# Kernel optimization log

Hardware: AMD Instinct MI355X
Metric: run time of the kernel (lower is better)

The kernel has to match this reference:

```python
import jax, jax.numpy as jnp
import numpy as np

B, LQ, LK, D = 16, 2048, 2048, 64
TEMPERATURE = 8.0


def setup_inputs() -> dict:
    key = jax.random.key(0)
    kq, kk, kv, kt, km = jax.random.split(key, 5)
    q = jax.random.normal(kq, (B, LQ, D), dtype=jnp.float32)
    k = jax.random.normal(kk, (B, LK, D), dtype=jnp.float32)
    v = jax.random.normal(kv, (B, LK, D), dtype=jnp.float32)
    # time differences are positive
    time_diff = jax.random.uniform(kt, (B, LQ, LK), dtype=jnp.float32)
    mask = jax.random.randint(km, (B, LQ, LK), 0, 2).astype(bool)
    time_plus_weight = jnp.zeros((1,), dtype=jnp.float32)
    time_mul_weight = jnp.ones((1,), dtype=jnp.float32)
    return {"q": q, "k": k, "v": v, "time_diff": time_diff, "mask": mask,
            "time_plus_weight": time_plus_weight, "time_mul_weight": time_mul_weight}


def reference(q, k, v, time_diff, mask, time_plus_weight, time_mul_weight):
    # attn = QK^T / temperature  -> [B, LQ, LK]
    attn = jnp.einsum("bqd,bkd->bqk", q, k) / TEMPERATURE
    # time-decay bias (global mean/max over the whole time_diff tensor)
    td = time_diff / jnp.mean(time_diff)
    td = td + jax.nn.softplus(time_plus_weight) * jnp.max(td)
    time_diff_weight = 1.0 / jnp.log(jnp.exp(jnp.float32(1.0)) + td)
    attn = attn + time_mul_weight * time_diff_weight
    attn = jnp.where(mask, jnp.float32(-1e10), attn)
    attn = jax.nn.softmax(attn, axis=2)
    # dropout is identity in eval / p-effective-0 reference
    output = jnp.einsum("bqk,bkd->bqd", attn, v)
    return (output, attn)
```

## Files before the change

kernel.cpp:

```cpp
#include <hip/hip_runtime.h>
#include <hip/hip_bf16.h>

#define B_N 16
#define LQ_N 2048
#define LK_N 2048
#define D_N 64

typedef __attribute__((ext_vector_type(8))) __bf16 bf16x8;
typedef __attribute__((ext_vector_type(4))) float f32x4;
typedef __attribute__((ext_vector_type(2))) unsigned u32x2;
typedef __attribute__((ext_vector_type(4))) unsigned u32x4;

__device__ __forceinline__ unsigned cvt_pk_bf16(float lo, float hi) {
  unsigned r;
  asm("v_cvt_pk_bf16_f32 %0, %1, %2" : "=v"(r) : "v"(lo), "v"(hi));
  return r;
}

__device__ __forceinline__ void gl_lds16(const float* g, float* l) {
  __builtin_amdgcn_global_load_lds(
      (const __attribute__((address_space(1))) void*)g,
      (__attribute__((address_space(3))) void*)l, 16, 0, 0);
}

#define WAIT_VMC(N)  do { asm volatile("s_waitcnt vmcnt(" #N ")" ::: "memory"); __builtin_amdgcn_sched_barrier(0); } while (0)
#define WAIT_LGKM0() do { asm volatile("s_waitcnt lgkmcnt(0)" ::: "memory");    __builtin_amdgcn_sched_barrier(0); } while (0)
#define SBAR()       __builtin_amdgcn_sched_barrier(0)

__global__ __launch_bounds__(256) void red1_kernel(const float* __restrict__ td,
                                                   float* __restrict__ ws) {
  const int tid = threadIdx.x;
  const int gid = blockIdx.x * 256 + tid;
  float s = 0.f, mx = -1e30f;
  const float4* p = reinterpret_cast<const float4*>(td);
  for (int i = gid; i < 16777216; i += 524288) {
    float4 x = p[i];
    s += (x.x + x.y) + (x.z + x.w);
    mx = fmaxf(mx, fmaxf(fmaxf(x.x, x.y), fmaxf(x.z, x.w)));
  }
#pragma unroll
  for (int m = 1; m < 64; m <<= 1) {
    s += __shfl_xor(s, m, 64);
    mx = fmaxf(mx, __shfl_xor(mx, m, 64));
  }
  __shared__ float ss[4], sm[4];
  if ((tid & 63) == 0) { ss[tid >> 6] = s; sm[tid >> 6] = mx; }
  __syncthreads();
  if (tid == 0) {
    ws[blockIdx.x]        = (ss[0] + ss[1]) + (ss[2] + ss[3]);
    ws[2048 + blockIdx.x] = fmaxf(fmaxf(sm[0], sm[1]), fmaxf(sm[2], sm[3]));
  }
}

__global__ __launch_bounds__(256) void red2_kernel(const float* __restrict__ tpw,
                                                   const unsigned* __restrict__ mku,
                                                   float* __restrict__ ws) {
  const int tid = threadIdx.x;
  double s = 0.0; float mx = -1e30f;
  for (int i = tid; i < 2048; i += 256) { s += (double)ws[i]; mx = fmaxf(mx, ws[2048 + i]); }
#pragma unroll
  for (int m = 1; m < 64; m <<= 1) {
    s += __shfl_xor(s, m, 64);
    mx = fmaxf(mx, __shfl_xor(mx, m, 64));
  }
  unsigned big = 0;
  for (int i = tid; i < 1024; i += 256) big |= (mku[i] > 1u) ? 1u : 0u;
  const int anyw = __any(big != 0);
  __shared__ double sd[4]; __shared__ float sm[4]; __shared__ int sa[4];
  if ((tid & 63) == 0) { sd[tid >> 6] = s; sm[tid >> 6] = mx; sa[tid >> 6] = anyw; }
  __syncthreads();
  if (tid == 0) {
    double tot = (sd[0] + sd[1]) + (sd[2] + sd[3]);
    float m4 = fmaxf(fmaxf(sm[0], sm[1]), fmaxf(sm[2], sm[3]));
    double mean = tot / 67108864.0;
    float inv_mean = (float)(1.0 / mean);
    float sp = log1pf(__expf(tpw[0]));
    ws[4096] = inv_mean;
    ws[4097] = sp * m4 * inv_mean;
    ws[4098] = (sa[0] | sa[1] | sa[2] | sa[3]) ? 1.f : 0.f;
    ws[4099] = 2.718281828459045f + sp * m4 * inv_mean;
  }
}

__global__ __launch_bounds__(1024)
void attn_kernel(
    const float* __restrict__ q, const float* __restrict__ kp, const float* __restrict__ vp,
    const float* __restrict__ td, const unsigned char* __restrict__ maskb,
    const float* __restrict__ tmwp, const float* __restrict__ ws,
    float* __restrict__ out, float* __restrict__ attn) {

  __shared__ float regA[16][2][1024];
  __shared__ unsigned short Qsb[16 * 72];
  __shared__ unsigned short Ps[16][16 * 24];
  __shared__ float rsum[16][16];

  const int tid  = threadIdx.x;
  const int w    = tid >> 6;
  const int lane = tid & 63;
  const int lrow = lane & 15;
  const int lgrp = lane >> 4;

  const int b     = blockIdx.x >> 7;
  const int qbase = (blockIdx.x & 127) << 4;

  const float inv_mean = ws[4096];
  const float ec       = ws[4099];
  const float tmw      = tmwp[0];
  const float sc       = tmw * 2.0813689810056077f;
  const int   msh      = (ws[4098] != 0.f) ? 0 : 2;

  if (tid < 256) {
    const float qscale = 0.18033688011112042f;
    const int row = tid >> 4, c4 = (tid & 15) << 2;
    f32x4 x = *reinterpret_cast<const f32x4*>(q + ((size_t)(b * LQ_N + qbase + row) << 6) + c4);
    *reinterpret_cast<u32x2*>(&Qsb[row * 72 + c4]) =
        u32x2{ cvt_pk_bf16(x[0] * qscale, x[1] * qscale),
               cvt_pk_bf16(x[2] * qscale, x[3] * qscale) };
  }
  __syncthreads();

  const unsigned qrow = (unsigned)(b * LQ_N + qbase + lrow);
  const unsigned tdo0 = (qrow << 11) + (unsigned)(w * 16 + lgrp * 4);
  const unsigned kvo0 = ((unsigned)b << 17) + ((unsigned)w << 10);
  const unsigned pA = (lgrp << 6) + ((lrow ^ lgrp)       << 2);
  const unsigned pB = (lgrp << 6) + ((lrow ^ (lgrp + 4)) << 2);

  auto dma16 = [&](const float* src_base, int c, int pb) {
    const unsigned base = kvo0 + (unsigned)c * 16384u;
    gl_lds16(src_base + (base         + pA), &regA[w][pb][0]);
    gl_lds16(src_base + (base +  256u + pB), &regA[w][pb][256]);
    gl_lds16(src_base + (base +  512u + pA), &regA[w][pb][512]);
    gl_lds16(src_base + (base +  768u + pB), &regA[w][pb][768]);
  };

  auto ldtd = [&](int c, f32x4* tdv, unsigned* mk4) {
    const unsigned to = tdo0 + (unsigned)c * 256u;
    *tdv = __builtin_nontemporal_load(reinterpret_cast<const f32x4*>(td + to));
    if (msh == 0) {
      *mk4 = *reinterpret_cast<const unsigned*>(maskb + to);
    } else {
      u32x4 m = __builtin_nontemporal_load(
          reinterpret_cast<const u32x4*>(maskb + ((size_t)to << 2)));
      *mk4 = (m[0] & 1u) | ((m[1] & 1u) << 8) | ((m[2] & 1u) << 16) | ((m[3] & 1u) << 24);
    }
  };

  dma16(kp, 0, 0); SBAR();
  dma16(kp, 1, 1); SBAR();
  f32x4    tdb[2];
  unsigned mkb[2];
  ldtd(0, &tdb[0], &mkb[0]); SBAR();

  float rs = 0.f;
  u32x2 E[8];

#pragma unroll
  for (int c = 0; c < 8; ++c) {
    if (c == 0)      { WAIT_VMC(5); }
    else if (c <= 6) { WAIT_VMC(6); }
    else             { WAIT_VMC(2); }

    f32x4 acc = {0.f, 0.f, 0.f, 0.f};
#pragma unroll
    for (int h = 0; h < 2; ++h) {
      const int g0 = (h * 8 + lgrp * 2 + 0) ^ (lrow & 7);
      const int g1 = (h * 8 + lgrp * 2 + 1) ^ (lrow & 7);
      f32x4 ka = *(const f32x4*)&regA[w][c & 1][lrow * 64 + g0 * 4];
      f32x4 kc = *(const f32x4*)&regA[w][c & 1][lrow * 64 + g1 * 4];
      bf16x8 qv = *(const bf16x8*)&Qsb[lrow * 72 + h * 32 + lgrp * 8];
      u32x4 kd = { cvt_pk_bf16(ka[0], ka[1]), cvt_pk_bf16(ka[2], ka[3]),
                   cvt_pk_bf16(kc[0], kc[1]), cvt_pk_bf16(kc[2], kc[3]) };
      acc = __builtin_amdgcn_mfma_f32_16x16x32_bf16(__builtin_bit_cast(bf16x8, kd), qv,
                                                    acc, 0, 0, 0);
    }
    WAIT_LGKM0();
    if (c < 6) { dma16(kp, c + 2, c & 1); SBAR(); }
    if (c < 7) { ldtd(c + 1, &tdb[(c + 1) & 1], &mkb[(c + 1) & 1]); SBAR(); }

    if (c <= 5)      { WAIT_VMC(5); }
    else if (c == 6) { WAIT_VMC(1); }
    else             { WAIT_VMC(0); }

    const f32x4    tv  = tdb[c & 1];
    const unsigned mk4 = mkb[c & 1];
    float e4[4];
#pragma unroll
    for (int i = 0; i < 4; ++i) {
      const float z  = __builtin_fmaf(tv[i], inv_mean, ec);
      const float l2 = __builtin_amdgcn_logf(z);
      const float r  = __builtin_amdgcn_rcpf(l2);
      const float sv = __builtin_fmaf(sc, r, acc[i]);
      const float e  = ((mk4 >> (8 * i)) & 0xffu) ? 0.f : __builtin_amdgcn_exp2f(sv);
      e4[i] = e;
      rs += e;
    }
    E[c] = u32x2{ cvt_pk_bf16(e4[0], e4[1]), cvt_pk_bf16(e4[2], e4[3]) };
  }

  dma16(vp, 0, 0); SBAR();
  dma16(vp, 1, 1); SBAR();

  rs += __shfl_xor(rs, 16, 64);
  rs += __shfl_xor(rs, 32, 64);
  if (lgrp == 0) rsum[w][lrow] = rs;
  __syncthreads();
  float invl;
  {
    float s = 0.f;
#pragma unroll
    for (int w2 = 0; w2 < 16; ++w2) s += rsum[w2][lrow];
    invl = __fdividef(1.f, s);
  }

  f32x4 oacc[4];
#pragma unroll
  for (int n = 0; n < 4; ++n) oacc[n] = {0.f, 0.f, 0.f, 0.f};

  const u32x4 zz = {0u, 0u, 0u, 0u};
#pragma unroll
  for (int c = 0; c < 8; ++c) {
    if (c == 0)      { WAIT_VMC(4); }
    else if (c == 1) { WAIT_VMC(5); }
    else if (c <= 6) { WAIT_VMC(6); }
    else             { WAIT_VMC(2); }

    const unsigned ex = E[c][0], ey = E[c][1];
    f32x4 pv;
    pv[0] = __uint_as_float(ex << 16)         * invl;
    pv[1] = __uint_as_float(ex & 0xffff0000u) * invl;
    pv[2] = __uint_as_float(ey << 16)         * invl;
    pv[3] = __uint_as_float(ey & 0xffff0000u) * invl;

    const unsigned d01 = cvt_pk_bf16(pv[0], pv[1]);
    const unsigned d23 = cvt_pk_bf16(pv[2], pv[3]);
    *reinterpret_cast<u32x2*>(&Ps[w][lrow * 24 + lgrp * 4]) = u32x2{ d01, d23 };

    bf16x8 pa;
    if (lgrp < 2) pa = *(const bf16x8*)&Ps[w][lrow * 24 + lgrp * 8];
    else          pa = __builtin_bit_cast(bf16x8, zz);

#pragma unroll
    for (int n = 0; n < 4; ++n) {
      u32x4 vd;
      if (lgrp < 2) {
        float vv[8];
#pragma unroll
        for (int e = 0; e < 8; ++e) {
          const int r    = lgrp * 8 + e;
          const int dcol = n * 16 + lrow;
          const int slot = (dcol >> 2) ^ (r & 7);
          vv[e] = regA[w][c & 1][r * 64 + slot * 4 + (dcol & 3)];
        }
        vd = u32x4{ cvt_pk_bf16(vv[0], vv[1]), cvt_pk_bf16(vv[2], vv[3]),
                    cvt_pk_bf16(vv[4], vv[5]), cvt_pk_bf16(vv[6], vv[7]) };
      } else {
        vd = zz;
      }
      oacc[n] = __builtin_amdgcn_mfma_f32_16x16x32_bf16(pa, __builtin_bit_cast(bf16x8, vd),
                                                        oacc[n], 0, 0, 0);
    }

    WAIT_LGKM0();
    if (c < 6) { dma16(vp, c + 2, c & 1); SBAR(); }

    __builtin_nontemporal_store(pv, reinterpret_cast<f32x4*>(attn + tdo0 + (unsigned)c * 256u));
  }

#pragma unroll
  for (int n = 0; n < 4; ++n)
#pragma unroll
    for (int i = 0; i < 4; ++i)
      regA[w][0][(lgrp * 4 + i) * 64 + n * 16 + lrow] = oacc[n][i];
  __syncthreads();
  {
    float s = 0.f;
#pragma unroll
    for (int w2 = 0; w2 < 16; ++w2) s += regA[w2][0][tid];
    out[((size_t)(b * LQ_N + qbase) << 6) + tid] = s;
  }
}

extern "C" void kernel_launch(void* const* d_in, const int* in_sizes, int n_in,
                              void* d_out, int out_size, void* d_ws, size_t ws_size,
                              hipStream_t stream) {
  const float* q   = (const float*)d_in[0];
  const float* k   = (const float*)d_in[1];
  const float* v   = (const float*)d_in[2];
  const float* td  = (const float*)d_in[3];
  const unsigned char* mask = (const unsigned char*)d_in[4];
  const float* tpw = (const float*)d_in[5];
  const float* tmw = (const float*)d_in[6];
  float* out  = (float*)d_out;
  float* attn = out + (size_t)B_N * LQ_N * D_N;
  float* wsf  = (float*)d_ws;

  red1_kernel<<<2048, 256, 0, stream>>>(td, wsf);
  red2_kernel<<<1, 256, 0, stream>>>(tpw, (const unsigned*)mask, wsf);
  attn_kernel<<<2048, 1024, 0, stream>>>(q, k, v, td, mask, tmw, wsf, out, attn);
}
```

Baseline: 360.5 us.

## Replace LDS DMA pipeline with register-prefetched K/V loads and LDS-staged E values

```diff
diff --git a/kernel.cpp b/kernel.cpp
--- a/kernel.cpp
+++ b/kernel.cpp
@@ -16,16 +16,6 @@
   asm("v_cvt_pk_bf16_f32 %0, %1, %2" : "=v"(r) : "v"(lo), "v"(hi));
   return r;
 }
-
-__device__ __forceinline__ void gl_lds16(const float* g, float* l) {
-  __builtin_amdgcn_global_load_lds(
-      (const __attribute__((address_space(1))) void*)g,
-      (__attribute__((address_space(3))) void*)l, 16, 0, 0);
-}
-
-#define WAIT_VMC(N)  do { asm volatile("s_waitcnt vmcnt(" #N ")" ::: "memory"); __builtin_amdgcn_sched_barrier(0); } while (0)
-#define WAIT_LGKM0() do { asm volatile("s_waitcnt lgkmcnt(0)" ::: "memory");    __builtin_amdgcn_sched_barrier(0); } while (0)
-#define SBAR()       __builtin_amdgcn_sched_barrier(0)
 
 __global__ __launch_bounds__(256) void red1_kernel(const float* __restrict__ td,
                                                    float* __restrict__ ws) {
@@ -76,7 +66,6 @@
     float inv_mean = (float)(1.0 / mean);
     float sp = log1pf(__expf(tpw[0]));
     ws[4096] = inv_mean;
-    ws[4097] = sp * m4 * inv_mean;
     ws[4098] = (sa[0] | sa[1] | sa[2] | sa[3]) ? 1.f : 0.f;
     ws[4099] = 2.718281828459045f + sp * m4 * inv_mean;
   }
@@ -89,8 +78,8 @@
     const float* __restrict__ tmwp, const float* __restrict__ ws,
     float* __restrict__ out, float* __restrict__ attn) {
 
-  __shared__ float regA[16][2][1024];
-  __shared__ unsigned short Qsb[16 * 72];
+  __shared__ u32x2 Elds[8192];
+  __shared__ float Vb[16][1024];
   __shared__ unsigned short Ps[16][16 * 24];
   __shared__ float rsum[16][16];
 
@@ -109,96 +98,80 @@
   const float sc       = tmw * 2.0813689810056077f;
   const int   msh      = (ws[4098] != 0.f) ? 0 : 2;
 
-  if (tid < 256) {
-    const float qscale = 0.18033688011112042f;
-    const int row = tid >> 4, c4 = (tid & 15) << 2;
-    f32x4 x = *reinterpret_cast<const f32x4*>(q + ((size_t)(b * LQ_N + qbase + row) << 6) + c4);
-    *reinterpret_cast<u32x2*>(&Qsb[row * 72 + c4]) =
-        u32x2{ cvt_pk_bf16(x[0] * qscale, x[1] * qscale),
-               cvt_pk_bf16(x[2] * qscale, x[3] * qscale) };
-  }
-  __syncthreads();
-
-  const unsigned qrow = (unsigned)(b * LQ_N + qbase + lrow);
-  const unsigned tdo0 = (qrow << 11) + (unsigned)(w * 16 + lgrp * 4);
-  const unsigned kvo0 = ((unsigned)b << 17) + ((unsigned)w << 10);
-  const unsigned pA = (lgrp << 6) + ((lrow ^ lgrp)       << 2);
-  const unsigned pB = (lgrp << 6) + ((lrow ^ (lgrp + 4)) << 2);
-
-  auto dma16 = [&](const float* src_base, int c, int pb) {
-    const unsigned base = kvo0 + (unsigned)c * 16384u;
-    gl_lds16(src_base + (base         + pA), &regA[w][pb][0]);
-    gl_lds16(src_base + (base +  256u + pB), &regA[w][pb][256]);
-    gl_lds16(src_base + (base +  512u + pA), &regA[w][pb][512]);
-    gl_lds16(src_base + (base +  768u + pB), &regA[w][pb][768]);
-  };
-
+  const unsigned qrow  = (unsigned)(b * LQ_N + qbase + lrow);
+  const unsigned tdo0  = (qrow << 11) + (unsigned)(w * 16 + lgrp * 4);
+  const unsigned kvo0  = ((unsigned)b << 17);
+
+  const float qscale = 0.18033688011112042f;
+  bf16x8 qa[2];
+  {
+    const float* qb = q + ((size_t)qrow << 6) + lgrp * 8;
+    f32x4 a0 = *reinterpret_cast<const f32x4*>(qb);
+    f32x4 a1 = *reinterpret_cast<const f32x4*>(qb + 4);
+    f32x4 a2 = *reinterpret_cast<const f32x4*>(qb + 32);
+    f32x4 a3 = *reinterpret_cast<const f32x4*>(qb + 36);
+    u32x4 k0 = { cvt_pk_bf16(a0[0]*qscale, a0[1]*qscale), cvt_pk_bf16(a0[2]*qscale, a0[3]*qscale),
+                 cvt_pk_bf16(a1[0]*qscale, a1[1]*qscale), cvt_pk_bf16(a1[2]*qscale, a1[3]*qscale) };
+    u32x4 k1 = { cvt_pk_bf16(a2[0]*qscale, a2[1]*qscale), cvt_pk_bf16(a2[2]*qscale, a2[3]*qscale),
+                 cvt_pk_bf16(a3[0]*qscale, a3[1]*qscale), cvt_pk_bf16(a3[2]*qscale, a3[3]*qscale) };
+    qa[0] = __builtin_bit_cast(bf16x8, k0);
+    qa[1] = __builtin_bit_cast(bf16x8, k1);
+  }
+
+  auto ldk = [&](int c, f32x4* kf) {
+    const float* kr = kp + kvo0 + (unsigned)((c * 256 + w * 16 + lrow) << 6) + lgrp * 8;
+    kf[0] = *reinterpret_cast<const f32x4*>(kr);
+    kf[1] = *reinterpret_cast<const f32x4*>(kr + 4);
+    kf[2] = *reinterpret_cast<const f32x4*>(kr + 32);
+    kf[3] = *reinterpret_cast<const f32x4*>(kr + 36);
+  };
   auto ldtd = [&](int c, f32x4* tdv, unsigned* mk4) {
     const unsigned to = tdo0 + (unsigned)c * 256u;
     *tdv = __builtin_nontemporal_load(reinterpret_cast<const f32x4*>(td + to));
     if (msh == 0) {
       *mk4 = *reinterpret_cast<const unsigned*>(maskb + to);
     } else {
-      u32x4 m = __builtin_nontemporal_load(
-          reinterpret_cast<const u32x4*>(maskb + ((size_t)to << 2)));
+      u32x4 m = *reinterpret_cast<const u32x4*>(maskb + ((size_t)to << 2));
       *mk4 = (m[0] & 1u) | ((m[1] & 1u) << 8) | ((m[2] & 1u) << 16) | ((m[3] & 1u) << 24);
     }
   };
 
-  dma16(kp, 0, 0); SBAR();
-  dma16(kp, 1, 1); SBAR();
-  f32x4    tdb[2];
-  unsigned mkb[2];
-  ldtd(0, &tdb[0], &mkb[0]); SBAR();
-
   float rs = 0.f;
-  u32x2 E[8];
-
-#pragma unroll
-  for (int c = 0; c < 8; ++c) {
-    if (c == 0)      { WAIT_VMC(5); }
-    else if (c <= 6) { WAIT_VMC(6); }
-    else             { WAIT_VMC(2); }
-
-    f32x4 acc = {0.f, 0.f, 0.f, 0.f};
-#pragma unroll
-    for (int h = 0; h < 2; ++h) {
-      const int g0 = (h * 8 + lgrp * 2 + 0) ^ (lrow & 7);
-      const int g1 = (h * 8 + lgrp * 2 + 1) ^ (lrow & 7);
-      f32x4 ka = *(const f32x4*)&regA[w][c & 1][lrow * 64 + g0 * 4];
-      f32x4 kc = *(const f32x4*)&regA[w][c & 1][lrow * 64 + g1 * 4];
-      bf16x8 qv = *(const bf16x8*)&Qsb[lrow * 72 + h * 32 + lgrp * 8];
-      u32x4 kd = { cvt_pk_bf16(ka[0], ka[1]), cvt_pk_bf16(ka[2], ka[3]),
-                   cvt_pk_bf16(kc[0], kc[1]), cvt_pk_bf16(kc[2], kc[3]) };
-      acc = __builtin_amdgcn_mfma_f32_16x16x32_bf16(__builtin_bit_cast(bf16x8, kd), qv,
-                                                    acc, 0, 0, 0);
-    }
-    WAIT_LGKM0();
-    if (c < 6) { dma16(kp, c + 2, c & 1); SBAR(); }
-    if (c < 7) { ldtd(c + 1, &tdb[(c + 1) & 1], &mkb[(c + 1) & 1]); SBAR(); }
-
-    if (c <= 5)      { WAIT_VMC(5); }
-    else if (c == 6) { WAIT_VMC(1); }
-    else             { WAIT_VMC(0); }
-
-    const f32x4    tv  = tdb[c & 1];
-    const unsigned mk4 = mkb[c & 1];
-    float e4[4];
-#pragma unroll
-    for (int i = 0; i < 4; ++i) {
-      const float z  = __builtin_fmaf(tv[i], inv_mean, ec);
-      const float l2 = __builtin_amdgcn_logf(z);
-      const float r  = __builtin_amdgcn_rcpf(l2);
-      const float sv = __builtin_fmaf(sc, r, acc[i]);
-      const float e  = ((mk4 >> (8 * i)) & 0xffu) ? 0.f : __builtin_amdgcn_exp2f(sv);
-      e4[i] = e;
-      rs += e;
-    }
-    E[c] = u32x2{ cvt_pk_bf16(e4[0], e4[1]), cvt_pk_bf16(e4[2], e4[3]) };
-  }
-
-  dma16(vp, 0, 0); SBAR();
-  dma16(vp, 1, 1); SBAR();
+  {
+    f32x4    kf[2][4];
+    f32x4    tdb[2];
+    unsigned mkb[2];
+    ldk(0, kf[0]);
+    ldtd(0, &tdb[0], &mkb[0]);
+#pragma unroll
+    for (int c = 0; c < 8; ++c) {
+      if (c < 7) { ldk(c + 1, kf[(c + 1) & 1]); ldtd(c + 1, &tdb[(c + 1) & 1], &mkb[(c + 1) & 1]); }
+
+      const f32x4* kc = kf[c & 1];
+      u32x4 kd0 = { cvt_pk_bf16(kc[0][0], kc[0][1]), cvt_pk_bf16(kc[0][2], kc[0][3]),
+                    cvt_pk_bf16(kc[1][0], kc[1][1]), cvt_pk_bf16(kc[1][2], kc[1][3]) };
+      u32x4 kd1 = { cvt_pk_bf16(kc[2][0], kc[2][1]), cvt_pk_bf16(kc[2][2], kc[2][3]),
+                    cvt_pk_bf16(kc[3][0], kc[3][1]), cvt_pk_bf16(kc[3][2], kc[3][3]) };
+      f32x4 acc = {0.f, 0.f, 0.f, 0.f};
+      acc = __builtin_amdgcn_mfma_f32_16x16x32_bf16(__builtin_bit_cast(bf16x8, kd0), qa[0], acc, 0, 0, 0);
+      acc = __builtin_amdgcn_mfma_f32_16x16x32_bf16(__builtin_bit_cast(bf16x8, kd1), qa[1], acc, 0, 0, 0);
+
+      const f32x4    tv  = tdb[c & 1];
+      const unsigned mk4 = mkb[c & 1];
+      float e4[4];
+#pragma unroll
+      for (int i = 0; i < 4; ++i) {
+        const float z  = __builtin_fmaf(tv[i], inv_mean, ec);
+        const float l2 = __builtin_amdgcn_logf(z);
+        const float r  = __builtin_amdgcn_rcpf(l2);
+        const float sv = __builtin_fmaf(sc, r, acc[i]);
+        const float e  = ((mk4 >> (8 * i)) & 0xffu) ? 0.f : __builtin_amdgcn_exp2f(sv);
+        e4[i] = e;
+        rs += e;
+      }
+      Elds[(c << 10) + tid] = u32x2{ cvt_pk_bf16(e4[0], e4[1]), cvt_pk_bf16(e4[2], e4[3]) };
+    }
+  }
 
   rs += __shfl_xor(rs, 16, 64);
   rs += __shfl_xor(rs, 32, 64);
@@ -212,70 +185,89 @@
     invl = __fdividef(1.f, s);
   }
 
+  auto ldv = [&](int c, f32x4* vr) {
+#pragma unroll
+    for (int t = 0; t < 4; ++t) {
+      const int r = t * 4 + lgrp;
+      vr[t] = *reinterpret_cast<const f32x4*>(
+          vp + kvo0 + (unsigned)((c * 256 + w * 16 + r) << 6) + lrow * 4);
+    }
+  };
+  auto stv = [&](const f32x4* vr) {
+#pragma unroll
+    for (int t = 0; t < 4; ++t) {
+      const int r    = t * 4 + lgrp;
+      const int slot = lrow ^ (r & 7);
+      *reinterpret_cast<f32x4*>(&Vb[w][r * 64 + slot * 4]) = vr[t];
+    }
+  };
+
   f32x4 oacc[4];
 #pragma unroll
   for (int n = 0; n < 4; ++n) oacc[n] = {0.f, 0.f, 0.f, 0.f};
-
   const u32x4 zz = {0u, 0u, 0u, 0u};
-#pragma unroll
-  for (int c = 0; c < 8; ++c) {
-    if (c == 0)      { WAIT_VMC(4); }
-    else if (c == 1) { WAIT_VMC(5); }
-    else if (c <= 6) { WAIT_VMC(6); }
-    else             { WAIT_VMC(2); }
-
-    const unsigned ex = E[c][0], ey = E[c][1];
-    f32x4 pv;
-    pv[0] = __uint_as_float(ex << 16)         * invl;
-    pv[1] = __uint_as_float(ex & 0xffff0000u) * invl;
-    pv[2] = __uint_as_float(ey << 16)         * invl;
-    pv[3] = __uint_as_float(ey & 0xffff0000u) * invl;
-
-    const unsigned d01 = cvt_pk_bf16(pv[0], pv[1]);
-    const unsigned d23 = cvt_pk_bf16(pv[2], pv[3]);
-    *reinterpret_cast<u32x2*>(&Ps[w][lrow * 24 + lgrp * 4]) = u32x2{ d01, d23 };
-
-    bf16x8 pa;
-    if (lgrp < 2) pa = *(const bf16x8*)&Ps[w][lrow * 24 + lgrp * 8];
-    else          pa = __builtin_bit_cast(bf16x8, zz);
-
-#pragma unroll
-    for (int n = 0; n < 4; ++n) {
-      u32x4 vd;
-      if (lgrp < 2) {
-        float vv[8];
-#pragma unroll
-        for (int e = 0; e < 8; ++e) {
-          const int r    = lgrp * 8 + e;
-          const int dcol = n * 16 + lrow;
-          const int slot = (dcol >> 2) ^ (r & 7);
-          vv[e] = regA[w][c & 1][r * 64 + slot * 4 + (dcol & 3)];
+
+  {
+    f32x4 vr[4];
+    ldv(0, vr);
+    stv(vr);
+#pragma unroll
+    for (int c = 0; c < 8; ++c) {
+      const u32x2 ee = Elds[(c << 10) + tid];
+      f32x4 pv;
+      pv[0] = __uint_as_float(ee[0] << 16)         * invl;
+      pv[1] = __uint_as_float(ee[0] & 0xffff0000u) * invl;
+      pv[2] = __uint_as_float(ee[1] << 16)         * invl;
+      pv[3] = __uint_as_float(ee[1] & 0xffff0000u) * invl;
+
+      __builtin_nontemporal_store(pv, reinterpret_cast<f32x4*>(attn + tdo0 + (unsigned)c * 256u));
+
+      const unsigned d01 = cvt_pk_bf16(pv[0], pv[1]);
+      const unsigned d23 = cvt_pk_bf16(pv[2], pv[3]);
+      *reinterpret_cast<u32x2*>(&Ps[w][lrow * 24 + lgrp * 4]) = u32x2{ d01, d23 };
+      bf16x8 pa;
+      if (lgrp < 2) pa = *(const bf16x8*)&Ps[w][lrow * 24 + lgrp * 8];
+      else          pa = __builtin_bit_cast(bf16x8, zz);
+
+      f32x4 vrN[4];
+      if (c < 7) ldv(c + 1, vrN);
+
+#pragma unroll
+      for (int n = 0; n < 4; ++n) {
+        u32x4 vd;
+        if (lgrp < 2) {
+          float vv[8];
+#pragma unroll
+          for (int e = 0; e < 8; ++e) {
+            const int r    = lgrp * 8 + e;
+            const int dcol = n * 16 + lrow;
+            const int slot = (dcol >> 2) ^ (r & 7);
+            vv[e] = Vb[w][r * 64 + slot * 4 + (dcol & 3)];
+          }
+          vd = u32x4{ cvt_pk_bf16(vv[0], vv[1]), cvt_pk_bf16(vv[2], vv[3]),
+                      cvt_pk_bf16(vv[4], vv[5]), cvt_pk_bf16(vv[6], vv[7]) };
+        } else {
+          vd = zz;
         }
-        vd = u32x4{ cvt_pk_bf16(vv[0], vv[1]), cvt_pk_bf16(vv[2], vv[3]),
-                    cvt_pk_bf16(vv[4], vv[5]), cvt_pk_bf16(vv[6], vv[7]) };
-      } else {
-        vd = zz;
+        oacc[n] = __builtin_amdgcn_mfma_f32_16x16x32_bf16(pa, __builtin_bit_cast(bf16x8, vd),
+                                                          oacc[n], 0, 0, 0);
       }
-      oacc[n] = __builtin_amdgcn_mfma_f32_16x16x32_bf16(pa, __builtin_bit_cast(bf16x8, vd),
-                                                        oacc[n], 0, 0, 0);
-    }
-
-    WAIT_LGKM0();
-    if (c < 6) { dma16(vp, c + 2, c & 1); SBAR(); }
-
-    __builtin_nontemporal_store(pv, reinterpret_cast<f32x4*>(attn + tdo0 + (unsigned)c * 256u));
-  }
-
+
+      if (c < 7) stv(vrN);
+    }
+  }
+
+  __syncthreads();
 #pragma unroll
   for (int n = 0; n < 4; ++n)
 #pragma unroll
     for (int i = 0; i < 4; ++i)
-      regA[w][0][(lgrp * 4 + i) * 64 + n * 16 + lrow] = oacc[n][i];
+      Vb[w][(lgrp * 4 + i) * 64 + n * 16 + lrow] = oacc[n][i];
   __syncthreads();
   {
     float s = 0.f;
 #pragma unroll
-    for (int w2 = 0; w2 < 16; ++w2) s += regA[w2][0][tid];
+    for (int w2 = 0; w2 < 16; ++w2) s += Vb[w2][tid];
     out[((size_t)(b * LQ_N + qbase) << 6) + tid] = s;
   }
 }
```

Result: slower. 406.5 us (+12.8%).
